# Optimization experiments

Hardware: AMD Instinct MI355X
Metric: run time of the kernel (lower is better)

Reference implementation:

```python
import jax, jax.numpy as jnp
import numpy as np

B, S, D, H = 4, 2048, 1024, 16
DH = D // H


def setup_inputs() -> dict:
    key = jax.random.key(0)
    k1, k2, k3, k4, k5 = jax.random.split(key, 5)
    X = jax.random.normal(k1, (B, S, D), dtype=jnp.float32)
    W1 = jax.random.normal(k2, (3 * D, D), dtype=jnp.float32) * 0.02
    b1 = jax.random.normal(k3, (3 * D,), dtype=jnp.float32) * 0.01
    W2 = jax.random.normal(k4, (D, D), dtype=jnp.float32) * 0.02
    b2 = jax.random.normal(k5, (D,), dtype=jnp.float32) * 0.01
    return {"X": X, "W1": W1, "b1": b1, "W2": W2, "b2": b2}


def reference(X, W1, b1, W2, b2):
    b, s, d = X.shape
    # fused QKV projection (nn.Linear: y = x @ W.T + b)
    Y = X @ W1.T + b1                                   # [B,S,3D]
    Q, K, V = jnp.split(Y, 3, axis=2)                   # each [B,S,D]
    # reshape(x): view (B,S,H,DH) then permute(0,2,3,1) -> [B,H,DH,S]
    q = Q.reshape(b, s, H, DH).transpose(0, 2, 3, 1)    # [B,H,DH,S]
    v = V.reshape(b, s, H, DH).transpose(0, 2, 3, 1)    # [B,H,DH,S]
    # reshape(x, k=True): permute(0,2,1,3) -> [B,H,S,DH]
    k = K.reshape(b, s, H, DH).transpose(0, 2, 1, 3)    # [B,H,S,DH]
    # w = q @ k / sqrt(q.size(-1)) ; note q.size(-1) == S in this layout
    w = jnp.einsum('bhds,bhse->bhde', q, k) / jnp.sqrt(jnp.asarray(s, X.dtype))  # [B,H,DH,DH]
    w = jax.nn.softmax(w, axis=-1)
    out = jnp.einsum('bhde,bhes->bhds', w, v)           # [B,H,DH,S]
    # cat(): raw contiguous view of [B,H,DH,S] into [B,S,H*DH] (memory-order reshape)
    out = out.reshape(b, s, H * DH)                     # [B,S,D]
    return out @ W2.T + b2
```

## Files before the change

### kernel.cpp

```cpp
#include <hip/hip_runtime.h>
#include <stdint.h>

#define B_ 4
#define S_ 2048
#define D_ 1024
#define H_ 16
#define DH_ 64
#define M_TOT (B_*S_)
#define N1_ (3*D_)
#define K_ D_
#define NCH 8

typedef __bf16 bf16_8 __attribute__((ext_vector_type(8)));
typedef float  f32x4  __attribute__((ext_vector_type(4)));
typedef unsigned short u16;

typedef __attribute__((address_space(1))) const void* gas_t;
typedef __attribute__((address_space(3))) void*       las_t;

__device__ __forceinline__ unsigned short f2bf(float f) {
    union { float f; unsigned u; } v; v.f = f;
    unsigned r = v.u + 0x7FFFu + ((v.u >> 16) & 1u);
    return (unsigned short)(r >> 16);
}

__device__ __forceinline__ void async_ld16(const void* g, void* l) {
    __builtin_amdgcn_global_load_lds((gas_t)g, (las_t)l, 16, 0, 0);
}

__global__ __launch_bounds__(256)
void cast_kernel(const float* __restrict__ X, const float* __restrict__ W1,
                 const float* __restrict__ W2, unsigned short* __restrict__ Xb,
                 unsigned short* __restrict__ W1b, unsigned short* __restrict__ W2b) {
    const int nX  = (M_TOT * K_) / 4;
    const int nW1 = (N1_ * K_) / 4;
    int i = blockIdx.x * 256 + threadIdx.x;
    const float4* src; unsigned short* dst; int j;
    if (i < nX)            { src = (const float4*)X;  dst = Xb;  j = i; }
    else if (i < nX + nW1) { src = (const float4*)W1; dst = W1b; j = i - nX; }
    else                   { src = (const float4*)W2; dst = W2b; j = i - nX - nW1; }
    float4 v = src[j];
    ushort4 o;
    o.x = f2bf(v.x); o.y = f2bf(v.y); o.z = f2bf(v.z); o.w = f2bf(v.w);
    ((ushort4*)dst)[j] = o;
}

template<int N, int NBX, int EPI>
__global__ __launch_bounds__(256)
void gemm_bt(const unsigned short* __restrict__ A,
             const unsigned short* __restrict__ Bm,
             const float* __restrict__ bias,
             void* __restrict__ C, int K,
             u16* __restrict__ QT, u16* __restrict__ KT, u16* __restrict__ VT) {
    __shared__ unsigned short As[128 * 64];
    __shared__ unsigned short Bs[128 * 64];
    const int t    = threadIdx.x;
    const int wid  = t >> 6;
    const int lane = t & 63;
    const int lrow = lane & 15;
    const int lq   = lane >> 4;

    const int lid  = blockIdx.y * NBX + blockIdx.x;
    const int xcd  = lid & 7;
    const int slot = lid >> 3;
    const int by   = xcd * (gridDim.y >> 3) + slot / NBX;
    const int bx   = slot % NBX;
    const int m0   = by * 128;
    const int n0   = bx * 128;

    const int inst  = by >> 3;
    const int hblk  = by & 7;
    const size_t arow0 = (size_t)((inst >> 1) * 1024 + hblk * 128);
    const int koff  = (inst & 1) * 1024;

    const int wm   = (wid >> 1) * 64;
    const int wn   = (wid & 1) * 64;

    f32x4 acc[4][4] = {};

    for (int k0 = 0; k0 < K; k0 += 64) {
#pragma unroll
        for (int p = 0; p < 4; p++) {
            const int c   = p * 256 + t;
            const int row = c >> 3;
            const int kb  = (c & 7) ^ (row & 7);
            if constexpr (EPI == 3)
                async_ld16(A + (arow0 + row) * (size_t)S_ + koff + k0 + kb * 8, (char*)As + c * 16);
            else
                async_ld16(A + (size_t)(m0 + row) * K + k0 + kb * 8, (char*)As + c * 16);
            async_ld16(Bm + (size_t)(n0 + row) * K + k0 + kb * 8, (char*)Bs + c * 16);
        }
        __syncthreads();

#pragma unroll
        for (int ks = 0; ks < 2; ks++) {
            bf16_8 af[4], bfr[4];
#pragma unroll
            for (int mt = 0; mt < 4; mt++) {
                const int r  = wm + mt * 16 + lrow;
                const int kb = (ks * 4 + lq) ^ (r & 7);
                af[mt] = *(const bf16_8*)(As + (r * 8 + kb) * 8);
            }
#pragma unroll
            for (int nt = 0; nt < 4; nt++) {
                const int r  = wn + nt * 16 + lrow;
                const int kb = (ks * 4 + lq) ^ (r & 7);
                bfr[nt] = *(const bf16_8*)(Bs + (r * 8 + kb) * 8);
            }
#pragma unroll
            for (int mt = 0; mt < 4; mt++)
#pragma unroll
                for (int nt = 0; nt < 4; nt++)
                    acc[mt][nt] = __builtin_amdgcn_mfma_f32_16x16x32_bf16(af[mt], bfr[nt], acc[mt][nt], 0, 0, 0);
        }
        __syncthreads();
    }

#pragma unroll
    for (int nt = 0; nt < 4; nt++) {
        const int col = n0 + wn + nt * 16 + lrow;
        const float bv = (EPI == 2) ? bias[col] : 0.f;
#pragma unroll
        for (int mt = 0; mt < 4; mt++) {
            const int row = m0 + wm + mt * 16 + lq * 4;
            f32x4 a = acc[mt][nt];
            if constexpr (EPI == 2) {
                ushort4 o;
                o.x = f2bf(a[0] + bv); o.y = f2bf(a[1] + bv);
                o.z = f2bf(a[2] + bv); o.w = f2bf(a[3] + bv);
                const int b = row >> 11, s = row & 2047;
                const int d = col & 63;
                if (col < 1024) {
                    *(ushort4*)(QT + ((size_t)(b * 16 + (col >> 6)) * 64 + d) * (size_t)S_ + s) = o;
                } else if (col < 2048) {
                    *(ushort4*)(KT + ((size_t)(b * 16 + ((col >> 6) - 16)) * 64 + d) * (size_t)S_ + s) = o;
                } else {
                    *(ushort4*)(VT + ((size_t)(b * 16 + ((col >> 6) - 32)) * 64 + d) * (size_t)S_ + s) = o;
                }
            } else {
                ushort4 o;
                o.x = f2bf(a[0]); o.y = f2bf(a[1]); o.z = f2bf(a[2]); o.w = f2bf(a[3]);
                u16* Cp = (u16*)C;
                *(ushort4*)(Cp + ((size_t)((row >> 10) * 16 + ((row >> 6) & 15)) * 1024 + col) * 64
                                + (row & 63)) = o;
            }
        }
    }
}

__global__ __launch_bounds__(256)
void attn_qk(const u16* __restrict__ QT, const u16* __restrict__ KT,
             float* __restrict__ Scp) {
    __shared__ u16 Qs[64 * 64];
    __shared__ u16 Ks[64 * 64];
    const int bh = blockIdx.x, ch = blockIdx.y;
    const int t = threadIdx.x, wid = t >> 6, lane = t & 63;
    const int lrow = lane & 15, lq = lane >> 4;
    const int wm2 = (wid >> 1) * 32, wn2 = (wid & 1) * 32;
    const u16* Qh = QT + (size_t)bh * 64 * S_;
    const u16* Kh = KT + (size_t)bh * 64 * S_;

    f32x4 acc[2][2] = {};
    for (int kt = 0; kt < 4; kt++) {
        const int s0 = ch * 256 + kt * 64;
#pragma unroll
        for (int p = 0; p < 4; p++) {
            const int c   = p * 256 + t;
            const int cc  = c & 511;
            const int row = cc >> 3;
            const int kb  = (cc & 7) ^ (row & 7);
            if (p < 2)
                async_ld16(Qh + (size_t)row * S_ + s0 + kb * 8, (char*)Qs + cc * 16);
            else
                async_ld16(Kh + (size_t)row * S_ + s0 + kb * 8, (char*)Ks + cc * 16);
        }
        __syncthreads();
#pragma unroll
        for (int ks = 0; ks < 2; ks++) {
            bf16_8 aq[2], bk[2];
#pragma unroll
            for (int mt = 0; mt < 2; mt++) {
                const int r  = wm2 + mt * 16 + lrow;
                const int kb = (ks * 4 + lq) ^ (r & 7);
                aq[mt] = *(const bf16_8*)(Qs + (r * 8 + kb) * 8);
            }
#pragma unroll
            for (int nt = 0; nt < 2; nt++) {
                const int r  = wn2 + nt * 16 + lrow;
                const int kb = (ks * 4 + lq) ^ (r & 7);
                bk[nt] = *(const bf16_8*)(Ks + (r * 8 + kb) * 8);
            }
#pragma unroll
            for (int mt = 0; mt < 2; mt++)
#pragma unroll
                for (int nt = 0; nt < 2; nt++)
                    acc[mt][nt] = __builtin_amdgcn_mfma_f32_16x16x32_bf16(aq[mt], bk[nt], acc[mt][nt], 0, 0, 0);
        }
        __syncthreads();
    }

    float* out = Scp + (size_t)(bh * NCH + ch) * 4096;
#pragma unroll
    for (int mt = 0; mt < 2; mt++)
#pragma unroll
        for (int nt = 0; nt < 2; nt++)
#pragma unroll
            for (int i = 0; i < 4; i++)
                out[(wm2 + mt * 16 + lq * 4 + i) * 64 + wn2 + nt * 16 + lrow] = acc[mt][nt][i];
}

__global__ __launch_bounds__(256)
void attn_softmax(const float* __restrict__ Scp, unsigned short* __restrict__ Wb) {
    const int bh = blockIdx.x;
    const int t = threadIdx.x;
    const int d = t >> 2, q = t & 3;
    float s[16] = {};
#pragma unroll
    for (int c = 0; c < NCH; c++) {
        const float4* p = (const float4*)(Scp + ((size_t)(bh * NCH + c) * 64 + d) * 64 + q * 16);
#pragma unroll
        for (int j = 0; j < 4; j++) {
            float4 v = p[j];
            s[j*4+0] += v.x; s[j*4+1] += v.y; s[j*4+2] += v.z; s[j*4+3] += v.w;
        }
    }
    const float scale = 0.022097086912079608f;
    float m = -3.0e38f;
#pragma unroll
    for (int i = 0; i < 16; i++) { s[i] *= scale; m = fmaxf(m, s[i]); }
    m = fmaxf(m, __shfl_xor(m, 1));
    m = fmaxf(m, __shfl_xor(m, 2));
    float sum = 0.f;
#pragma unroll
    for (int i = 0; i < 16; i++) { s[i] = __expf(s[i] - m); sum += s[i]; }
    sum += __shfl_xor(sum, 1);
    sum += __shfl_xor(sum, 2);
    const float inv = 1.0f / sum;
    unsigned short* w = Wb + (size_t)bh * 4096 + d * 64 + q * 16;
    ushort4 o0, o1, o2, o3;
    o0.x=f2bf(s[0]*inv);  o0.y=f2bf(s[1]*inv);  o0.z=f2bf(s[2]*inv);  o0.w=f2bf(s[3]*inv);
    o1.x=f2bf(s[4]*inv);  o1.y=f2bf(s[5]*inv);  o1.z=f2bf(s[6]*inv);  o1.w=f2bf(s[7]*inv);
    o2.x=f2bf(s[8]*inv);  o2.y=f2bf(s[9]*inv);  o2.z=f2bf(s[10]*inv); o2.w=f2bf(s[11]*inv);
    o3.x=f2bf(s[12]*inv); o3.y=f2bf(s[13]*inv); o3.z=f2bf(s[14]*inv); o3.w=f2bf(s[15]*inv);
    ((ushort4*)w)[0]=o0; ((ushort4*)w)[1]=o1; ((ushort4*)w)[2]=o2; ((ushort4*)w)[3]=o3;
}

__global__ __launch_bounds__(256)
void gemm_light(const u16* __restrict__ Wb, const u16* __restrict__ VWT,
                const float* __restrict__ b2, float* __restrict__ out) {
    __shared__ u16 Ws[64 * 64];
    __shared__ u16 Vs[256 * 64];
    const int bx = blockIdx.x, byy = blockIdx.y;
    const int n0 = bx * 128;
    const int b = byy >> 4, h = byy & 15;
    const int t = threadIdx.x, wid = t >> 6, lane = t & 63;
    const int lrow = lane & 15, lq = lane >> 4;
    const int wsl = wid >> 1;
    const int wn  = wid & 1;

#pragma unroll
    for (int j = 0; j < 2; j++) {
        const int c = j * 256 + t;
        const int row = c >> 3, kb = (c & 7) ^ (row & 7);
        async_ld16(Wb + (size_t)byy * 4096 + row * 64 + kb * 8, (char*)Ws + c * 16);
    }
#pragma unroll
    for (int p = 0; p < 8; p++) {
        const int c = p * 256 + t;
        const int slice = c >> 10, rowc = (c >> 3) & 127;
        const int kb = (c & 7) ^ (rowc & 7);
        async_ld16(VWT + ((size_t)((b * 2 + slice) * 16 + h) * 1024 + n0 + rowc) * 64 + kb * 8,
                   (char*)Vs + c * 16);
    }
    __syncthreads();

    f32x4 acc[4][4] = {};
#pragma unroll
    for (int ks = 0; ks < 2; ks++) {
        bf16_8 af[4], bfr[4];
#pragma unroll
        for (int mt = 0; mt < 4; mt++) {
            const int r  = mt * 16 + lrow;
            const int kb = (ks * 4 + lq) ^ (r & 7);
            af[mt] = *(const bf16_8*)(Ws + (r * 8 + kb) * 8);
        }
#pragma unroll
        for (int nt = 0; nt < 4; nt++) {
            const int rn = wn * 64 + nt * 16 + lrow;
            const int kb = (ks * 4 + lq) ^ (rn & 7);
            bfr[nt] = *(const bf16_8*)(Vs + ((wsl * 128 + rn) * 8 + kb) * 8);
        }
#pragma unroll
        for (int mt = 0; mt < 4; mt++)
#pragma unroll
            for (int nt = 0; nt < 4; nt++)
                acc[mt][nt] = __builtin_amdgcn_mfma_f32_16x16x32_bf16(af[mt], bfr[nt], acc[mt][nt], 0, 0, 0);
    }

    float* op = out + (size_t)byy * 128 * 1024;
#pragma unroll
    for (int nt = 0; nt < 4; nt++) {
        const int col = n0 + wn * 64 + nt * 16 + lrow;
        const float bv = b2[col];
#pragma unroll
        for (int mt = 0; mt < 4; mt++)
#pragma unroll
            for (int i = 0; i < 4; i++) {
                const int d = mt * 16 + lq * 4 + i;
                op[(size_t)(2 * d + wsl) * 1024 + col] = acc[mt][nt][i] + bv;
            }
    }
}

extern "C" void kernel_launch(void* const* d_in, const int* in_sizes, int n_in,
                              void* d_out, int out_size, void* d_ws, size_t ws_size,
                              hipStream_t stream) {
    const float* X  = (const float*)d_in[0];
    const float* W1 = (const float*)d_in[1];
    const float* b1 = (const float*)d_in[2];
    const float* W2 = (const float*)d_in[3];
    const float* b2 = (const float*)d_in[4];

    char* ws = (char*)d_ws;
    unsigned short* Xb  = (unsigned short*)(ws + 0);
    unsigned short* W1b = (unsigned short*)(ws + (16u << 20));
    unsigned short* W2b = (unsigned short*)(ws + (22u << 20));
    unsigned short* QT  = (unsigned short*)(ws + (24u << 20));
    unsigned short* KT  = (unsigned short*)(ws + (40u << 20));
    unsigned short* VT  = (unsigned short*)(ws + (56u << 20));
    unsigned short* Wb  = (unsigned short*)(ws + 0);
    unsigned short* VWT = (unsigned short*)(ws + (1u << 20));
    float* Scp = (float*)d_out;

    cast_kernel<<<12288, 256, 0, stream>>>(X, W1, W2, Xb, W1b, W2b);
    gemm_bt<N1_, N1_/128, 2><<<dim3(N1_ / 128, M_TOT / 128), 256, 0, stream>>>(
        Xb, W1b, b1, nullptr, K_, QT, KT, VT);
    attn_qk<<<dim3(64, NCH), 256, 0, stream>>>(QT, KT, Scp);
    attn_softmax<<<64, 256, 0, stream>>>(Scp, Wb);
    gemm_bt<D_, D_/128, 3><<<dim3(D_ / 128, M_TOT / 128), 256, 0, stream>>>(
        VT, W2b, b2, VWT, K_, nullptr, nullptr, nullptr);
    gemm_light<<<dim3(8, 64), 256, 0, stream>>>(Wb, VWT, b2, (float*)d_out);
}
```

Before: 217.2 us.

## Reorder attention tail to compute softmax-weighted V before output projection

Replaces the V·W2-first path (a large GEMM on transposed V plus a light per-head GEMM applying the softmax weights) with a per-head attn_pv kernel computing W@V into a bf16 buffer, followed by a standard GEMM with W2 and bias writing fp32 output directly. V is now stored in [b,h,s,e] layout from the QKV epilogue using scalar strided stores. This simplifies the projection GEMM's addressing and removes the gemm_light pass, but adds uncoalesced scalar stores for V and for the attention output.

```diff
diff --git a/kernel.cpp b/kernel.cpp
--- a/kernel.cpp
+++ b/kernel.cpp
@@ -51,7 +51,7 @@
              const unsigned short* __restrict__ Bm,
              const float* __restrict__ bias,
              void* __restrict__ C, int K,
-             u16* __restrict__ QT, u16* __restrict__ KT, u16* __restrict__ VT) {
+             u16* __restrict__ QT, u16* __restrict__ KT, u16* __restrict__ Vh) {
     __shared__ unsigned short As[128 * 64];
     __shared__ unsigned short Bs[128 * 64];
     const int t    = threadIdx.x;
@@ -68,11 +68,6 @@
     const int m0   = by * 128;
     const int n0   = bx * 128;
 
-    const int inst  = by >> 3;
-    const int hblk  = by & 7;
-    const size_t arow0 = (size_t)((inst >> 1) * 1024 + hblk * 128);
-    const int koff  = (inst & 1) * 1024;
-
     const int wm   = (wid >> 1) * 64;
     const int wn   = (wid & 1) * 64;
 
@@ -84,10 +79,7 @@
             const int c   = p * 256 + t;
             const int row = c >> 3;
             const int kb  = (c & 7) ^ (row & 7);
-            if constexpr (EPI == 3)
-                async_ld16(A + (arow0 + row) * (size_t)S_ + koff + k0 + kb * 8, (char*)As + c * 16);
-            else
-                async_ld16(A + (size_t)(m0 + row) * K + k0 + kb * 8, (char*)As + c * 16);
+            async_ld16(A  + (size_t)(m0 + row) * K + k0 + kb * 8, (char*)As + c * 16);
             async_ld16(Bm + (size_t)(n0 + row) * K + k0 + kb * 8, (char*)Bs + c * 16);
         }
         __syncthreads();
@@ -119,7 +111,7 @@
 #pragma unroll
     for (int nt = 0; nt < 4; nt++) {
         const int col = n0 + wn + nt * 16 + lrow;
-        const float bv = (EPI == 2) ? bias[col] : 0.f;
+        const float bv = bias[col];
 #pragma unroll
         for (int mt = 0; mt < 4; mt++) {
             const int row = m0 + wm + mt * 16 + lq * 4;
@@ -135,14 +127,18 @@
                 } else if (col < 2048) {
                     *(ushort4*)(KT + ((size_t)(b * 16 + ((col >> 6) - 16)) * 64 + d) * (size_t)S_ + s) = o;
                 } else {
-                    *(ushort4*)(VT + ((size_t)(b * 16 + ((col >> 6) - 32)) * 64 + d) * (size_t)S_ + s) = o;
+                    const int h = (col >> 6) - 32, e = col & 63;
+                    u16* vp = Vh + ((size_t)(b * 16 + h) * S_ + s) * 64 + e;
+                    vp[0]   = o.x;
+                    vp[64]  = o.y;
+                    vp[128] = o.z;
+                    vp[192] = o.w;
                 }
             } else {
-                ushort4 o;
-                o.x = f2bf(a[0]); o.y = f2bf(a[1]); o.z = f2bf(a[2]); o.w = f2bf(a[3]);
-                u16* Cp = (u16*)C;
-                *(ushort4*)(Cp + ((size_t)((row >> 10) * 16 + ((row >> 6) & 15)) * 1024 + col) * 64
-                                + (row & 63)) = o;
+                float* Cp = (float*)C;
+#pragma unroll
+                for (int i = 0; i < 4; i++)
+                    Cp[(size_t)(row + i) * N + col] = a[i] + bv;
             }
         }
     }
@@ -246,31 +242,27 @@
 }
 
 __global__ __launch_bounds__(256)
-void gemm_light(const u16* __restrict__ Wb, const u16* __restrict__ VWT,
-                const float* __restrict__ b2, float* __restrict__ out) {
+void attn_pv(const u16* __restrict__ Wb, const u16* __restrict__ Vh,
+             u16* __restrict__ O) {
     __shared__ u16 Ws[64 * 64];
     __shared__ u16 Vs[256 * 64];
-    const int bx = blockIdx.x, byy = blockIdx.y;
-    const int n0 = bx * 128;
-    const int b = byy >> 4, h = byy & 15;
+    const int bh = blockIdx.x, sc = blockIdx.y;
     const int t = threadIdx.x, wid = t >> 6, lane = t & 63;
     const int lrow = lane & 15, lq = lane >> 4;
-    const int wsl = wid >> 1;
-    const int wn  = wid & 1;
+    const u16* Wh = Wb + (size_t)bh * 4096;
+    const u16* Vp = Vh + ((size_t)bh * S_ + sc * 256) * 64;
 
 #pragma unroll
     for (int j = 0; j < 2; j++) {
         const int c = j * 256 + t;
         const int row = c >> 3, kb = (c & 7) ^ (row & 7);
-        async_ld16(Wb + (size_t)byy * 4096 + row * 64 + kb * 8, (char*)Ws + c * 16);
+        async_ld16(Wh + row * 64 + kb * 8, (char*)Ws + c * 16);
     }
 #pragma unroll
     for (int p = 0; p < 8; p++) {
         const int c = p * 256 + t;
-        const int slice = c >> 10, rowc = (c >> 3) & 127;
-        const int kb = (c & 7) ^ (rowc & 7);
-        async_ld16(VWT + ((size_t)((b * 2 + slice) * 16 + h) * 1024 + n0 + rowc) * 64 + kb * 8,
-                   (char*)Vs + c * 16);
+        const int row = c >> 3, kb = (c & 7) ^ (row & 7);
+        async_ld16(Vp + (size_t)row * 64 + kb * 8, (char*)Vs + c * 16);
     }
     __syncthreads();
 
@@ -286,9 +278,9 @@
         }
 #pragma unroll
         for (int nt = 0; nt < 4; nt++) {
-            const int rn = wn * 64 + nt * 16 + lrow;
-            const int kb = (ks * 4 + lq) ^ (rn & 7);
-            bfr[nt] = *(const bf16_8*)(Vs + ((wsl * 128 + rn) * 8 + kb) * 8);
+            const int r  = wid * 64 + nt * 16 + lrow;
+            const int kb = (ks * 4 + lq) ^ (r & 7);
+            bfr[nt] = *(const bf16_8*)(Vs + (r * 8 + kb) * 8);
         }
 #pragma unroll
         for (int mt = 0; mt < 4; mt++)
@@ -297,19 +289,18 @@
                 acc[mt][nt] = __builtin_amdgcn_mfma_f32_16x16x32_bf16(af[mt], bfr[nt], acc[mt][nt], 0, 0, 0);
     }
 
-    float* op = out + (size_t)byy * 128 * 1024;
-#pragma unroll
-    for (int nt = 0; nt < 4; nt++) {
-        const int col = n0 + wn * 64 + nt * 16 + lrow;
-        const float bv = b2[col];
-#pragma unroll
-        for (int mt = 0; mt < 4; mt++)
-#pragma unroll
-            for (int i = 0; i < 4; i++) {
-                const int d = mt * 16 + lq * 4 + i;
-                op[(size_t)(2 * d + wsl) * 1024 + col] = acc[mt][nt][i] + bv;
-            }
-    }
+    const size_t obase = (size_t)bh * (DH_ * S_);
+    const int s0 = sc * 256 + wid * 64;
+#pragma unroll
+    for (int mt = 0; mt < 4; mt++)
+#pragma unroll
+        for (int nt = 0; nt < 4; nt++) {
+            const int d = mt * 16 + lq * 4;
+            const int s = s0 + nt * 16 + lrow;
+#pragma unroll
+            for (int i = 0; i < 4; i++)
+                O[obase + (size_t)(d + i) * S_ + s] = f2bf(acc[mt][nt][i]);
+        }
 }
 
 extern "C" void kernel_launch(void* const* d_in, const int* in_sizes, int n_in,
@@ -327,17 +318,17 @@
     unsigned short* W2b = (unsigned short*)(ws + (22u << 20));
     unsigned short* QT  = (unsigned short*)(ws + (24u << 20));
     unsigned short* KT  = (unsigned short*)(ws + (40u << 20));
-    unsigned short* VT  = (unsigned short*)(ws + (56u << 20));
+    unsigned short* Vh  = (unsigned short*)(ws + (56u << 20));
     unsigned short* Wb  = (unsigned short*)(ws + 0);
-    unsigned short* VWT = (unsigned short*)(ws + (1u << 20));
+    unsigned short* Ob  = (unsigned short*)(ws + (1u << 20));
     float* Scp = (float*)d_out;
 
     cast_kernel<<<12288, 256, 0, stream>>>(X, W1, W2, Xb, W1b, W2b);
     gemm_bt<N1_, N1_/128, 2><<<dim3(N1_ / 128, M_TOT / 128), 256, 0, stream>>>(
-        Xb, W1b, b1, nullptr, K_, QT, KT, VT);
+        Xb, W1b, b1, nullptr, K_, QT, KT, Vh);
     attn_qk<<<dim3(64, NCH), 256, 0, stream>>>(QT, KT, Scp);
     attn_softmax<<<64, 256, 0, stream>>>(Scp, Wb);
-    gemm_bt<D_, D_/128, 3><<<dim3(D_ / 128, M_TOT / 128), 256, 0, stream>>>(
-        VT, W2b, b2, VWT, K_, nullptr, nullptr, nullptr);
-    gemm_light<<<dim3(8, 64), 256, 0, stream>>>(Wb, VWT, b2, (float*)d_out);
-}
+    attn_pv<<<dim3(64, NCH), 256, 0, stream>>>(Wb, Vh, Ob);
+    gemm_bt<D_, D_/128, 0><<<dim3(D_ / 128, M_TOT / 128), 256, 0, stream>>>(
+        Ob, W2b, b2, d_out, K_, nullptr, nullptr, nullptr);
+}
```

Result: faster. 204.0 us (-6.1%).
